# Optimization experiments

Measured on AMD Instinct MI355X. Metric: run time of the kernel, lower is better.

The kernel has to match this reference:

```python
import jax, jax.numpy as jnp
import numpy as np

B, S, D = 4, 2048, 1024
HEADS, KEY_SIZE, SIZE_PER_HEAD = 16, 64, 64
OUT_DIM = HEADS * SIZE_PER_HEAD
NEG_BIG = 1e10


def setup_inputs() -> dict:
    key = jax.random.key(0)
    ks = jax.random.split(key, 6)
    q_value = jax.random.normal(ks[0], (B, S, D), dtype=jnp.float32)
    k_value = jax.random.normal(ks[1], (B, S, D), dtype=jnp.float32)
    v_value = jax.random.normal(ks[2], (B, S, D), dtype=jnp.float32)
    v_mask = jnp.ones((B, S, 1), dtype=jnp.float32)
    q_mask = jnp.ones((B, S, 1), dtype=jnp.float32)
    scale = 1.0 / np.sqrt(D)
    Wq = jax.random.normal(ks[3], (D, HEADS * KEY_SIZE), dtype=jnp.float32) * scale
    Wk = jax.random.normal(ks[4], (D, HEADS * KEY_SIZE), dtype=jnp.float32) * scale
    Wv = jax.random.normal(ks[5], (D, OUT_DIM), dtype=jnp.float32) * scale
    return {"q_value": q_value, "k_value": k_value, "v_value": v_value,
            "v_mask": v_mask, "q_mask": q_mask, "Wq": Wq, "Wk": Wk, "Wv": Wv}


def reference(q_value, k_value, v_value, v_mask, q_mask, Wq, Wk, Wv):
    b, sq, _ = q_value.shape
    sk = k_value.shape[1]
    # projections (no bias) -> [B, S, H, dh]
    qw = (q_value @ Wq).reshape(b, sq, HEADS, KEY_SIZE)
    kw = (k_value @ Wk).reshape(b, sk, HEADS, KEY_SIZE)
    vw = (v_value @ Wv).reshape(b, sk, HEADS, SIZE_PER_HEAD)
    # scores [B, H, Sq, Sk], scaled by sqrt(key_size)
    scores = jnp.einsum('bqhd,bkhd->bhqk', qw, kw) / jnp.sqrt(
        jnp.asarray(KEY_SIZE, dtype=qw.dtype))
    # additive key-side mask: v_mask [B, Sk, 1] -> broadcast over heads/queries
    scores = scores - (1.0 - v_mask[:, None, None, :, 0]) * NEG_BIG
    attn = jax.nn.softmax(scores, axis=-1)
    out = jnp.einsum('bhqk,bkhd->bqhd', attn, vw).reshape(b, sq, OUT_DIM)
    # multiplicative query-side mask
    return out * q_mask
```

## Files before the change

kernel.cpp:

```cpp
#include <hip/hip_runtime.h>

typedef __bf16 bf16_t;
typedef __bf16 bf16x8 __attribute__((ext_vector_type(8)));
typedef __bf16 bf16x4 __attribute__((ext_vector_type(4)));
typedef __bf16 bf16x2 __attribute__((ext_vector_type(2)));
typedef float  f32x4  __attribute__((ext_vector_type(4)));
typedef float  f32x16 __attribute__((ext_vector_type(16)));
typedef unsigned int u32x4 __attribute__((ext_vector_type(4)));
typedef int i32x2 __attribute__((ext_vector_type(2)));

#define MFMA16(A, B, C) __builtin_amdgcn_mfma_f32_16x16x32_bf16((A), (B), (C), 0, 0, 0)
#define MFMA32(A, B, C) __builtin_amdgcn_mfma_f32_32x32x16_bf16((A), (B), (C), 0, 0, 0)

constexpr int BB = 4;
constexpr int SS = 2048;
constexpr int DD = 1024;
constexpr int HH = 16;
constexpr int DH = 64;
constexpr float C1 = 0.18033688011112042f;

__device__ __forceinline__ void async_copy16(const void* g, void* l) {
    __builtin_amdgcn_global_load_lds(
        (const __attribute__((address_space(1))) void*)g,
        (__attribute__((address_space(3))) void*)l, 16, 0, 0);
}

__device__ __forceinline__ unsigned pack_bf16(float lo, float hi) {
    bf16x2 t;
    t[0] = (bf16_t)lo;
    t[1] = (bf16_t)hi;
    return __builtin_bit_cast(unsigned, t);
}

__device__ __forceinline__ void permswap(unsigned& a, unsigned& b) {
    i32x2 r = __builtin_amdgcn_permlane32_swap((int)a, (int)b, false, false);
    a = (unsigned)r[0];
    b = (unsigned)r[1];
}

__global__ __launch_bounds__(256) void conv_kernel(
    const float* __restrict__ q, const float* __restrict__ k,
    const float* __restrict__ v, bf16_t* __restrict__ outb)
{
    const float* src = blockIdx.z == 0 ? q : blockIdx.z == 1 ? k : v;
    bf16_t* dst = outb + ((size_t)blockIdx.z << 23);
    size_t i = ((size_t)blockIdx.x * 256 + threadIdx.x) * 8;
    f32x4 a = *(const f32x4*)&src[i];
    f32x4 b = *(const f32x4*)&src[i + 4];
    bf16x8 o;
    o[0] = (bf16_t)a[0]; o[1] = (bf16_t)a[1]; o[2] = (bf16_t)a[2]; o[3] = (bf16_t)a[3];
    o[4] = (bf16_t)b[0]; o[5] = (bf16_t)b[1]; o[6] = (bf16_t)b[2]; o[7] = (bf16_t)b[3];
    *(bf16x8*)&dst[i] = o;
}

__global__ __launch_bounds__(256) void wtrans_kernel(
    const float* __restrict__ Wq, const float* __restrict__ Wk,
    const float* __restrict__ Wv, bf16_t* __restrict__ Wt)
{
    const float* W = blockIdx.z == 0 ? Wq : blockIdx.z == 1 ? Wk : Wv;
    bf16_t* T = Wt + ((size_t)blockIdx.z << 20);

    __shared__ __align__(16) bf16_t tile[64][72];

    const int k0 = blockIdx.x * 64;
    const int n0 = blockIdx.y * 64;
    const int tid = threadIdx.x;

    #pragma unroll
    for (int i = 0; i < 4; i++) {
        int idx = tid + i * 256;
        int kk = idx >> 4;
        int nn = (idx & 15) * 4;
        f32x4 w = *(const f32x4*)&W[(size_t)(k0 + kk) * 1024 + n0 + nn];
        tile[nn + 0][kk] = (bf16_t)w[0];
        tile[nn + 1][kk] = (bf16_t)w[1];
        tile[nn + 2][kk] = (bf16_t)w[2];
        tile[nn + 3][kk] = (bf16_t)w[3];
    }
    __syncthreads();
    #pragma unroll
    for (int i = 0; i < 2; i++) {
        int idx = tid + i * 256;
        int nn = idx >> 3;
        int kk = (idx & 7) * 8;
        *(bf16x8*)&T[(size_t)(n0 + nn) * 1024 + k0 + kk] =
            *(const bf16x8*)&tile[nn][kk];
    }
}

__global__ __launch_bounds__(256) void proj_kernel(
    const bf16_t* __restrict__ Ab, const bf16_t* __restrict__ Wt,
    bf16_t* __restrict__ qw, bf16_t* __restrict__ kw, bf16_t* __restrict__ vwt)
{
    const int which = blockIdx.z;
    const bf16_t* A = Ab + ((size_t)which << 23);
    const bf16_t* T = Wt + ((size_t)which << 20);

    __shared__ bf16_t Alds[128 * 64];
    __shared__ bf16_t Blds[128 * 64];

    const int tid = threadIdx.x;
    const int lane = tid & 63;
    const int wave = tid >> 6;
    const int quad = lane >> 4;
    const int l16 = lane & 15;

    const int id = blockIdx.x;
    const int xg = id & 7;
    const int sl = id >> 3;
    const int m0 = (((xg << 3) | (sl >> 3))) * 128;
    const int n0 = (sl & 7) * 128;

    const int wm = (wave >> 1) * 64;
    const int wn = (wave & 1) * 64;

    const int srow = lane >> 3;
    const int schk = lane & 7;

    f32x4 zero4 = {0.f, 0.f, 0.f, 0.f};
    f32x4 acc[4][4];
    #pragma unroll
    for (int i = 0; i < 4; i++)
        #pragma unroll
        for (int j = 0; j < 4; j++) acc[i][j] = zero4;

    for (int k0 = 0; k0 < DD; k0 += 64) {
        #pragma unroll
        for (int j = 0; j < 4; j++) {
            int r0 = wave * 32 + j * 8;
            int row = r0 + srow;
            int c = schk ^ (row & 7);
            async_copy16(&A[(size_t)(m0 + row) * 1024 + k0 + c * 8], &Alds[r0 * 64]);
        }
        #pragma unroll
        for (int j = 0; j < 4; j++) {
            int r0 = wave * 32 + j * 8;
            int row = r0 + srow;
            int c = schk ^ (row & 7);
            async_copy16(&T[(size_t)(n0 + row) * 1024 + k0 + c * 8], &Blds[r0 * 64]);
        }
        __syncthreads();

        #pragma unroll
        for (int s = 0; s < 2; s++) {
            bf16x8 af[4], bfr[4];
            #pragma unroll
            for (int mi = 0; mi < 4; mi++)
                af[mi] = *(const bf16x8*)&Alds[(wm + mi * 16 + l16) * 64 +
                             (((s * 4 + quad) ^ (l16 & 7)) << 3)];
            #pragma unroll
            for (int ni = 0; ni < 4; ni++)
                bfr[ni] = *(const bf16x8*)&Blds[(wn + ni * 16 + l16) * 64 +
                              (((s * 4 + quad) ^ (l16 & 7)) << 3)];
            #pragma unroll
            for (int mi = 0; mi < 4; mi++)
                #pragma unroll
                for (int ni = 0; ni < 4; ni++)
                    acc[mi][ni] = MFMA16(af[mi], bfr[ni], acc[mi][ni]);
        }
        __syncthreads();
    }

    if (which < 2) {
        bf16_t* Cout = which == 0 ? qw : kw;
        #pragma unroll
        for (int mi = 0; mi < 4; mi++)
            #pragma unroll
            for (int ni = 0; ni < 4; ni++)
                #pragma unroll
                for (int r = 0; r < 4; r++) {
                    int row = m0 + wm + mi * 16 + quad * 4 + r;
                    int col = n0 + wn + ni * 16 + l16;
                    Cout[(size_t)row * 1024 + col] = (bf16_t)acc[mi][ni][r];
                }
    } else {
        #pragma unroll
        for (int mi = 0; mi < 4; mi++)
            #pragma unroll
            for (int ni = 0; ni < 4; ni++) {
                int s0 = m0 + wm + mi * 16 + quad * 4;
                int col = n0 + wn + ni * 16 + l16;
                int b = s0 >> 11, s = s0 & 2047;
                int h = col >> 6, d = col & 63;
                bf16x4 p;
                p[0] = (bf16_t)acc[mi][ni][0]; p[1] = (bf16_t)acc[mi][ni][1];
                p[2] = (bf16_t)acc[mi][ni][2]; p[3] = (bf16_t)acc[mi][ni][3];
                *(bf16x4*)&vwt[(((size_t)((b * HH + h) * DH + d)) << 11) + s] = p;
            }
    }
}

__global__ __launch_bounds__(256) void attn_kernel(
    const bf16_t* __restrict__ qw, const bf16_t* __restrict__ kw,
    const bf16_t* __restrict__ vwt, const float* __restrict__ v_mask,
    const float* __restrict__ q_mask, float* __restrict__ out)
{
    const int linear = blockIdx.x;
    const int xg = linear & 7;
    const int sl = linear >> 3;
    const int grp = (xg << 3) | (sl >> 4);
    const int qt = sl & 15;
    const int b = grp >> 4;
    const int h = grp & 15;

    __shared__ __align__(16) bf16_t KV[4 * 4096];
    __shared__ float vml[2][64];

    const int tid = threadIdx.x;
    const int lane = tid & 63;
    const int wave = tid >> 6;
    const int l5 = lane & 31;
    const int hi = lane >> 5;
    const int q0 = qt * 128 + wave * 32;

    const int srow = lane >> 3;
    const int schk = lane & 7;

    bf16x8 qf[4];
    #pragma unroll
    for (int c = 0; c < 4; ++c)
        qf[c] = *(const bf16x8*)&qw[(size_t)(b * SS + q0 + l5) * 1024 + h * 64 +
                                    c * 16 + hi * 8];

    f32x16 zero16;
    #pragma unroll
    for (int i = 0; i < 16; ++i) zero16[i] = 0.f;

    const int vkh = (l5 & 7) ^ hi;
    const bf16_t* pj[4];
    #pragma unroll
    for (int j = 0; j < 4; ++j)
        pj[j] = &KV[l5 * 64 + ((vkh ^ (2 * j)) << 3)];
    const float* vmlp = &vml[0][hi * 4];

    const bf16_t* gk[2];
    const bf16_t* gv[2];
    #pragma unroll
    for (int j = 0; j < 2; ++j) {
        int row = (wave * 2 + j) * 8 + srow;
        int ck = schk ^ (row & 7);
        gk[j] = &kw[(size_t)(b * SS + row) * 1024 + h * 64 + ck * 8];
        gv[j] = &vwt[(((size_t)((b * HH + h) * DH + row)) << 11) + ck * 8];
    }
    const float* vmp = v_mask + b * SS + tid;

    auto stage = [&](int bi) {
        #pragma unroll
        for (int j = 0; j < 2; ++j) {
            async_copy16(gk[j], &KV[bi * 4096 + (wave * 2 + j) * 512]);
            gk[j] += 64 * 1024;
        }
        #pragma unroll
        for (int j = 0; j < 2; ++j) {
            async_copy16(gv[j], &KV[8192 + bi * 4096 + (wave * 2 + j) * 512]);
            gv[j] += 64;
        }
        if (tid < 64)
            vml[bi][tid] = (1.0f - *vmp) * 1.4426950408889634e10f;
        vmp += 64;
    };

    stage(0);
    __syncthreads();

    f32x16 o0 = zero16, o1 = zero16;
    f32x4 l4 = {0.f, 0.f, 0.f, 0.f};

    for (int t2 = 0; t2 < 32; t2 += 2) {
        #pragma unroll
        for (int cur = 0; cur < 2; ++cur) {
            if (t2 + cur + 1 < 32) stage(cur ^ 1);

            __builtin_amdgcn_s_setprio(1);
            f32x16 st0, st1;
            {
                bf16x8 k0 = *(const bf16x8*)(pj[0] + cur * 4096);
                bf16x8 k1 = *(const bf16x8*)(pj[0] + cur * 4096 + 2048);
                st0 = MFMA32(k0, qf[0], zero16);
                st1 = MFMA32(k1, qf[0], zero16);
            }
            #pragma unroll
            for (int c = 1; c < 4; ++c) {
                bf16x8 k0 = *(const bf16x8*)(pj[c] + cur * 4096);
                bf16x8 k1 = *(const bf16x8*)(pj[c] + cur * 4096 + 2048);
                st0 = MFMA32(k0, qf[c], st0);
                st1 = MFMA32(k1, qf[c], st1);
            }
            __builtin_amdgcn_s_setprio(0);

            #pragma unroll
            for (int kb = 0; kb < 2; ++kb) {
                f32x16& st = kb ? st1 : st0;
                #pragma unroll
                for (int g = 0; g < 4; ++g) {
                    f32x4 vm4 = *(const f32x4*)(vmlp + cur * 64 + kb * 32 + g * 8);
                    #pragma unroll
                    for (int j = 0; j < 4; ++j) {
                        float p = __builtin_amdgcn_exp2f(
                            __builtin_fmaf(st[g * 4 + j], C1, -vm4[j]));
                        st[g * 4 + j] = p;
                        l4[j] += p;
                    }
                }
                unsigned a0 = pack_bf16(st[0],  st[1]);
                unsigned a1 = pack_bf16(st[2],  st[3]);
                unsigned a2 = pack_bf16(st[4],  st[5]);
                unsigned a3 = pack_bf16(st[6],  st[7]);
                unsigned a4 = pack_bf16(st[8],  st[9]);
                unsigned a5 = pack_bf16(st[10], st[11]);
                unsigned a6 = pack_bf16(st[12], st[13]);
                unsigned a7 = pack_bf16(st[14], st[15]);
                permswap(a0, a2);
                permswap(a1, a3);
                permswap(a4, a6);
                permswap(a5, a7);
                u32x4 w0 = {a0, a1, a2, a3};
                u32x4 w1 = {a4, a5, a6, a7};
                bf16x8 bp0 = __builtin_bit_cast(bf16x8, w0);
                bf16x8 bp1 = __builtin_bit_cast(bf16x8, w1);

                __builtin_amdgcn_s_setprio(1);
                #pragma unroll
                for (int c = 0; c < 2; ++c) {
                    bf16x8 bp = c ? bp1 : bp0;
                    const bf16_t* pv = pj[kb * 2 + c] + 8192 + cur * 4096;
                    bf16x8 av0 = *(const bf16x8*)(pv);
                    bf16x8 av1 = *(const bf16x8*)(pv + 2048);
                    o0 = MFMA32(av0, bp, o0);
                    o1 = MFMA32(av1, bp, o1);
                }
                __builtin_amdgcn_s_setprio(0);
            }
            __syncthreads();
        }
    }

    float l_i = (l4[0] + l4[1]) + (l4[2] + l4[3]);
    l_i += __shfl_xor(l_i, 32);

    const int q = q0 + l5;
    const float sc = q_mask[b * SS + q] / l_i;
    #pragma unroll
    for (int db = 0; db < 2; ++db) {
        const f32x16 oa = db ? o1 : o0;
        #pragma unroll
        for (int g = 0; g < 4; ++g) {
            f32x4 o4;
            o4[0] = oa[g * 4 + 0] * sc;
            o4[1] = oa[g * 4 + 1] * sc;
            o4[2] = oa[g * 4 + 2] * sc;
            o4[3] = oa[g * 4 + 3] * sc;
            *(f32x4*)&out[(size_t)(b * SS + q) * 1024 + h * 64 +
                          db * 32 + g * 8 + hi * 4] = o4;
        }
    }
}

extern "C" void kernel_launch(void* const* d_in, const int* in_sizes, int n_in,
                              void* d_out, int out_size, void* d_ws, size_t ws_size,
                              hipStream_t stream)
{
    const float* q  = (const float*)d_in[0];
    const float* k  = (const float*)d_in[1];
    const float* v  = (const float*)d_in[2];
    const float* vm = (const float*)d_in[3];
    const float* qm = (const float*)d_in[4];
    const float* Wq = (const float*)d_in[5];
    const float* Wk = (const float*)d_in[6];
    const float* Wv = (const float*)d_in[7];
    float* out = (float*)d_out;

    const size_t elems = (size_t)BB * SS * DD;
    bf16_t* Ab  = (bf16_t*)d_ws;
    bf16_t* qw  = Ab + 3 * elems;
    bf16_t* kw  = qw + elems;
    bf16_t* vwt = kw + elems;
    bf16_t* Wt  = vwt + elems;

    conv_kernel<<<dim3(4096, 1, 3), 256, 0, stream>>>(q, k, v, Ab);
    wtrans_kernel<<<dim3(16, 16, 3), 256, 0, stream>>>(Wq, Wk, Wv, Wt);
    proj_kernel<<<dim3(512, 1, 3), 256, 0, stream>>>(Ab, Wt, qw, kw, vwt);
    attn_kernel<<<dim3(1024, 1, 1), 256, 0, stream>>>(qw, kw, vwt, vm, qm, out);
}
```

Before: 317.0 us.

## Shrink attention blocks to two waves with single-buffered staggered K/V staging

The attention kernel now runs 128-thread blocks covering 64 queries each, so the grid doubles to 2048 blocks. The double-buffered K/V tiles become single K and V buffers, which halves shared memory per block. V is loaded while QK^T and exp run, and the next K is loaded while PV runs, with two barriers per tile. The aim is higher occupancy and smaller LDS per block, at the cost of less K/V reuse per block, twice the global K/V traffic, and extra synchronisation.

```diff
diff --git a/kernel.cpp b/kernel.cpp
--- a/kernel.cpp
+++ b/kernel.cpp
@@ -190,7 +190,7 @@
     }
 }
 
-__global__ __launch_bounds__(256) void attn_kernel(
+__global__ __launch_bounds__(128) void attn_kernel(
     const bf16_t* __restrict__ qw, const bf16_t* __restrict__ kw,
     const bf16_t* __restrict__ vwt, const float* __restrict__ v_mask,
     const float* __restrict__ q_mask, float* __restrict__ out)
@@ -198,12 +198,12 @@
     const int linear = blockIdx.x;
     const int xg = linear & 7;
     const int sl = linear >> 3;
-    const int grp = (xg << 3) | (sl >> 4);
-    const int qt = sl & 15;
+    const int grp = (xg << 3) | (sl >> 5);
+    const int qt = sl & 31;
     const int b = grp >> 4;
     const int h = grp & 15;
 
-    __shared__ __align__(16) bf16_t KV[4 * 4096];
+    __shared__ __align__(16) bf16_t KV[2 * 4096];
     __shared__ float vml[2][64];
 
     const int tid = threadIdx.x;
@@ -211,7 +211,7 @@
     const int wave = tid >> 6;
     const int l5 = lane & 31;
     const int hi = lane >> 5;
-    const int q0 = qt * 128 + wave * 32;
+    const int q0 = qt * 64 + wave * 32;
 
     const int srow = lane >> 3;
     const int schk = lane & 7;
@@ -233,34 +233,33 @@
         pj[j] = &KV[l5 * 64 + ((vkh ^ (2 * j)) << 3)];
     const float* vmlp = &vml[0][hi * 4];
 
-    const bf16_t* gk[2];
-    const bf16_t* gv[2];
-    #pragma unroll
-    for (int j = 0; j < 2; ++j) {
-        int row = (wave * 2 + j) * 8 + srow;
-        int ck = schk ^ (row & 7);
-        gk[j] = &kw[(size_t)(b * SS + row) * 1024 + h * 64 + ck * 8];
-        gv[j] = &vwt[(((size_t)((b * HH + h) * DH + row)) << 11) + ck * 8];
-    }
+    const int ck = schk ^ srow;
+    const bf16_t* gk = &kw[(size_t)(b * SS + wave * 32 + srow) * 1024 +
+                           h * 64 + ck * 8];
+    const bf16_t* gv = &vwt[(((size_t)((b * HH + h) * DH + wave * 32 + srow)) << 11) +
+                            ck * 8];
     const float* vmp = v_mask + b * SS + tid;
 
-    auto stage = [&](int bi) {
-        #pragma unroll
-        for (int j = 0; j < 2; ++j) {
-            async_copy16(gk[j], &KV[bi * 4096 + (wave * 2 + j) * 512]);
-            gk[j] += 64 * 1024;
-        }
-        #pragma unroll
-        for (int j = 0; j < 2; ++j) {
-            async_copy16(gv[j], &KV[8192 + bi * 4096 + (wave * 2 + j) * 512]);
-            gv[j] += 64;
-        }
+    auto stageK = [&]() {
+        #pragma unroll
+        for (int j = 0; j < 4; ++j)
+            async_copy16(gk + j * 8192, &KV[(wave * 32 + j * 8) * 64]);
+        gk += 64 * 1024;
+    };
+    auto stageV = [&]() {
+        #pragma unroll
+        for (int j = 0; j < 4; ++j)
+            async_copy16(gv + j * 16384, &KV[4096 + (wave * 32 + j * 8) * 64]);
+        gv += 64;
+    };
+    auto stageVml = [&](int bi) {
         if (tid < 64)
             vml[bi][tid] = (1.0f - *vmp) * 1.4426950408889634e10f;
         vmp += 64;
     };
 
-    stage(0);
+    stageK();
+    stageVml(0);
     __syncthreads();
 
     f32x16 o0 = zero16, o1 = zero16;
@@ -269,20 +268,21 @@
     for (int t2 = 0; t2 < 32; t2 += 2) {
         #pragma unroll
         for (int cur = 0; cur < 2; ++cur) {
-            if (t2 + cur + 1 < 32) stage(cur ^ 1);
+            const int t = t2 + cur;
+            stageV();
 
             __builtin_amdgcn_s_setprio(1);
             f32x16 st0, st1;
             {
-                bf16x8 k0 = *(const bf16x8*)(pj[0] + cur * 4096);
-                bf16x8 k1 = *(const bf16x8*)(pj[0] + cur * 4096 + 2048);
+                bf16x8 k0 = *(const bf16x8*)(pj[0]);
+                bf16x8 k1 = *(const bf16x8*)(pj[0] + 2048);
                 st0 = MFMA32(k0, qf[0], zero16);
                 st1 = MFMA32(k1, qf[0], zero16);
             }
             #pragma unroll
             for (int c = 1; c < 4; ++c) {
-                bf16x8 k0 = *(const bf16x8*)(pj[c] + cur * 4096);
-                bf16x8 k1 = *(const bf16x8*)(pj[c] + cur * 4096 + 2048);
+                bf16x8 k0 = *(const bf16x8*)(pj[c]);
+                bf16x8 k1 = *(const bf16x8*)(pj[c] + 2048);
                 st0 = MFMA32(k0, qf[c], st0);
                 st1 = MFMA32(k1, qf[c], st1);
             }
@@ -302,6 +302,18 @@
                         l4[j] += p;
                     }
                 }
+            }
+
+            __syncthreads();
+
+            if (t < 31) {
+                stageK();
+                stageVml((cur ^ 1) & 1);
+            }
+
+            #pragma unroll
+            for (int kb = 0; kb < 2; ++kb) {
+                f32x16& st = kb ? st1 : st0;
                 unsigned a0 = pack_bf16(st[0],  st[1]);
                 unsigned a1 = pack_bf16(st[2],  st[3]);
                 unsigned a2 = pack_bf16(st[4],  st[5]);
@@ -323,7 +335,7 @@
                 #pragma unroll
                 for (int c = 0; c < 2; ++c) {
                     bf16x8 bp = c ? bp1 : bp0;
-                    const bf16_t* pv = pj[kb * 2 + c] + 8192 + cur * 4096;
+                    const bf16_t* pv = pj[kb * 2 + c] + 4096;
                     bf16x8 av0 = *(const bf16x8*)(pv);
                     bf16x8 av1 = *(const bf16x8*)(pv + 2048);
                     o0 = MFMA32(av0, bp, o0);
@@ -331,6 +343,7 @@
                 }
                 __builtin_amdgcn_s_setprio(0);
             }
+
             __syncthreads();
         }
     }
@@ -380,5 +393,5 @@
     conv_kernel<<<dim3(4096, 1, 3), 256, 0, stream>>>(q, k, v, Ab);
     wtrans_kernel<<<dim3(16, 16, 3), 256, 0, stream>>>(Wq, Wk, Wv, Wt);
     proj_kernel<<<dim3(512, 1, 3), 256, 0, stream>>>(Ab, Wt, qw, kw, vwt);
-    attn_kernel<<<dim3(1024, 1, 1), 256, 0, stream>>>(qw, kw, vwt, vm, qm, out);
-}
+    attn_kernel<<<dim3(2048, 1, 1), 128, 0, stream>>>(qw, kw, vwt, vm, qm, out);
+}
```

Result: slower. 349.1 us (+10.1%).

## Split attention waves into query-pair by key-half groups with LDS reduction

Applied to the files above, without the earlier changes.

Each wave now owns 64 queries (two 32-row blocks) and one 32-key half of every KV tile, instead of 32 queries over all keys. Each K fragment is reused for two query blocks, which halves LDS reads per MFMA. The per-wave partial outputs and row sums are combined through LDS at the end. The v_mask is now read straight from global inside the loop instead of being staged into shared memory. The cost is more accumulator registers (four f32x16 plus two Q sets) and an extra reduction and sync in the epilogue, which may lower occupancy.

```diff
diff --git a/kernel.cpp b/kernel.cpp
--- a/kernel.cpp
+++ b/kernel.cpp
@@ -18,6 +18,7 @@
 constexpr int HH = 16;
 constexpr int DH = 64;
 constexpr float C1 = 0.18033688011112042f;
+constexpr float C2 = 1.4426950408889634e10f;
 
 __device__ __forceinline__ void async_copy16(const void* g, void* l) {
     __builtin_amdgcn_global_load_lds(
@@ -36,6 +37,25 @@
     i32x2 r = __builtin_amdgcn_permlane32_swap((int)a, (int)b, false, false);
     a = (unsigned)r[0];
     b = (unsigned)r[1];
+}
+
+__device__ __forceinline__ void packP(const f32x16& st, bf16x8& w0, bf16x8& w1) {
+    unsigned a0 = pack_bf16(st[0],  st[1]);
+    unsigned a1 = pack_bf16(st[2],  st[3]);
+    unsigned a2 = pack_bf16(st[4],  st[5]);
+    unsigned a3 = pack_bf16(st[6],  st[7]);
+    unsigned a4 = pack_bf16(st[8],  st[9]);
+    unsigned a5 = pack_bf16(st[10], st[11]);
+    unsigned a6 = pack_bf16(st[12], st[13]);
+    unsigned a7 = pack_bf16(st[14], st[15]);
+    permswap(a0, a2);
+    permswap(a1, a3);
+    permswap(a4, a6);
+    permswap(a5, a7);
+    u32x4 u0 = {a0, a1, a2, a3};
+    u32x4 u1 = {a4, a5, a6, a7};
+    w0 = __builtin_bit_cast(bf16x8, u0);
+    w1 = __builtin_bit_cast(bf16x8, u1);
 }
 
 __global__ __launch_bounds__(256) void conv_kernel(
@@ -204,154 +224,176 @@
     const int h = grp & 15;
 
     __shared__ __align__(16) bf16_t KV[4 * 4096];
-    __shared__ float vml[2][64];
+    __shared__ float lred[2][2][64];
 
     const int tid = threadIdx.x;
     const int lane = tid & 63;
     const int wave = tid >> 6;
+    const int qg = wave >> 1;
+    const int kh = wave & 1;
     const int l5 = lane & 31;
     const int hi = lane >> 5;
-    const int q0 = qt * 128 + wave * 32;
+    const int q0 = qt * 128 + qg * 64;
 
     const int srow = lane >> 3;
     const int schk = lane & 7;
-
-    bf16x8 qf[4];
+    const int ck = schk ^ srow;
+
+    bf16x8 qf[2][4];
+    #pragma unroll
+    for (int qb = 0; qb < 2; ++qb)
+        #pragma unroll
+        for (int c = 0; c < 4; ++c)
+            qf[qb][c] = *(const bf16x8*)&qw[(size_t)(b * SS + q0 + qb * 32 + l5) * 1024 +
+                                            h * 64 + c * 16 + hi * 8];
+
+    f32x16 zero16;
+    #pragma unroll
+    for (int i = 0; i < 16; ++i) zero16[i] = 0.f;
+
+    const int vkh = (l5 & 7) ^ hi;
+    const bf16_t* pk[4];
     #pragma unroll
     for (int c = 0; c < 4; ++c)
-        qf[c] = *(const bf16x8*)&qw[(size_t)(b * SS + q0 + l5) * 1024 + h * 64 +
-                                    c * 16 + hi * 8];
-
-    f32x16 zero16;
-    #pragma unroll
-    for (int i = 0; i < 16; ++i) zero16[i] = 0.f;
-
-    const int vkh = (l5 & 7) ^ hi;
-    const bf16_t* pj[4];
-    #pragma unroll
-    for (int j = 0; j < 4; ++j)
-        pj[j] = &KV[l5 * 64 + ((vkh ^ (2 * j)) << 3)];
-    const float* vmlp = &vml[0][hi * 4];
-
-    const bf16_t* gk[2];
-    const bf16_t* gv[2];
-    #pragma unroll
-    for (int j = 0; j < 2; ++j) {
-        int row = (wave * 2 + j) * 8 + srow;
-        int ck = schk ^ (row & 7);
-        gk[j] = &kw[(size_t)(b * SS + row) * 1024 + h * 64 + ck * 8];
-        gv[j] = &vwt[(((size_t)((b * HH + h) * DH + row)) << 11) + ck * 8];
-    }
-    const float* vmp = v_mask + b * SS + tid;
+        pk[c] = &KV[kh * 2048 + l5 * 64 + ((vkh ^ (2 * c)) << 3)];
+    const bf16_t* pv[2];
+    #pragma unroll
+    for (int ks = 0; ks < 2; ++ks)
+        pv[ks] = &KV[8192 + l5 * 64 + ((vkh ^ (4 * kh) ^ (2 * ks)) << 3)];
+
+    const bf16_t* gk = &kw[(size_t)(b * SS + wave * 16 + srow) * 1024 + h * 64 + ck * 8];
+    const bf16_t* gv = &vwt[(((size_t)((b * HH + h) * DH + wave * 16 + srow)) << 11) +
+                            ck * 8];
+    const float* pvm = v_mask + b * SS + kh * 32 + hi * 4;
 
     auto stage = [&](int bi) {
         #pragma unroll
-        for (int j = 0; j < 2; ++j) {
-            async_copy16(gk[j], &KV[bi * 4096 + (wave * 2 + j) * 512]);
-            gk[j] += 64 * 1024;
-        }
-        #pragma unroll
-        for (int j = 0; j < 2; ++j) {
-            async_copy16(gv[j], &KV[8192 + bi * 4096 + (wave * 2 + j) * 512]);
-            gv[j] += 64;
-        }
-        if (tid < 64)
-            vml[bi][tid] = (1.0f - *vmp) * 1.4426950408889634e10f;
-        vmp += 64;
+        for (int j = 0; j < 2; ++j)
+            async_copy16(gk + j * 8192, &KV[bi * 4096 + (wave * 16 + j * 8) * 64]);
+        gk += 64 * 1024;
+        #pragma unroll
+        for (int j = 0; j < 2; ++j)
+            async_copy16(gv + j * 16384, &KV[8192 + bi * 4096 + (wave * 16 + j * 8) * 64]);
+        gv += 64;
     };
 
     stage(0);
     __syncthreads();
 
-    f32x16 o0 = zero16, o1 = zero16;
-    f32x4 l4 = {0.f, 0.f, 0.f, 0.f};
+    f32x16 o00 = zero16, o01 = zero16, o10 = zero16, o11 = zero16;
+    f32x4 la = {0.f, 0.f, 0.f, 0.f};
+    f32x4 lb = {0.f, 0.f, 0.f, 0.f};
 
     for (int t2 = 0; t2 < 32; t2 += 2) {
         #pragma unroll
         for (int cur = 0; cur < 2; ++cur) {
-            if (t2 + cur + 1 < 32) stage(cur ^ 1);
+            const int t = t2 + cur;
+
+            f32x4 vm4[4];
+            #pragma unroll
+            for (int g = 0; g < 4; ++g)
+                vm4[g] = *(const f32x4*)(pvm + g * 8);
+            pvm += 64;
+
+            if (t < 31) stage(cur ^ 1);
 
             __builtin_amdgcn_s_setprio(1);
             f32x16 st0, st1;
             {
-                bf16x8 k0 = *(const bf16x8*)(pj[0] + cur * 4096);
-                bf16x8 k1 = *(const bf16x8*)(pj[0] + cur * 4096 + 2048);
-                st0 = MFMA32(k0, qf[0], zero16);
-                st1 = MFMA32(k1, qf[0], zero16);
+                bf16x8 kf = *(const bf16x8*)(pk[0] + cur * 4096);
+                st0 = MFMA32(kf, qf[0][0], zero16);
+                st1 = MFMA32(kf, qf[1][0], zero16);
             }
             #pragma unroll
             for (int c = 1; c < 4; ++c) {
-                bf16x8 k0 = *(const bf16x8*)(pj[c] + cur * 4096);
-                bf16x8 k1 = *(const bf16x8*)(pj[c] + cur * 4096 + 2048);
-                st0 = MFMA32(k0, qf[c], st0);
-                st1 = MFMA32(k1, qf[c], st1);
+                bf16x8 kf = *(const bf16x8*)(pk[c] + cur * 4096);
+                st0 = MFMA32(kf, qf[0][c], st0);
+                st1 = MFMA32(kf, qf[1][c], st1);
             }
             __builtin_amdgcn_s_setprio(0);
 
             #pragma unroll
-            for (int kb = 0; kb < 2; ++kb) {
-                f32x16& st = kb ? st1 : st0;
+            for (int g = 0; g < 4; ++g) {
+                #pragma unroll
+                for (int j = 0; j < 4; ++j) {
+                    float nv = __builtin_fmaf(vm4[g][j], C2, -C2);
+                    float p0 = __builtin_amdgcn_exp2f(
+                        __builtin_fmaf(st0[g * 4 + j], C1, nv));
+                    st0[g * 4 + j] = p0;
+                    la[j] += p0;
+                    float p1 = __builtin_amdgcn_exp2f(
+                        __builtin_fmaf(st1[g * 4 + j], C1, nv));
+                    st1[g * 4 + j] = p1;
+                    lb[j] += p1;
+                }
+            }
+
+            bf16x8 bp00, bp01, bp10, bp11;
+            packP(st0, bp00, bp01);
+            packP(st1, bp10, bp11);
+
+            __builtin_amdgcn_s_setprio(1);
+            #pragma unroll
+            for (int ks = 0; ks < 2; ++ks) {
+                bf16x8 bpa = ks ? bp01 : bp00;
+                bf16x8 bpb = ks ? bp11 : bp10;
+                bf16x8 av0 = *(const bf16x8*)(pv[ks] + cur * 4096);
+                bf16x8 av1 = *(const bf16x8*)(pv[ks] + cur * 4096 + 2048);
+                o00 = MFMA32(av0, bpa, o00);
+                o10 = MFMA32(av0, bpb, o10);
+                o01 = MFMA32(av1, bpa, o01);
+                o11 = MFMA32(av1, bpb, o11);
+            }
+            __builtin_amdgcn_s_setprio(0);
+
+            __syncthreads();
+        }
+    }
+
+    float ls0 = (la[0] + la[1]) + (la[2] + la[3]);
+    float ls1 = (lb[0] + lb[1]) + (lb[2] + lb[3]);
+    float* R = (float*)KV;
+
+    if (kh == 1) {
+        *(f32x16*)&R[((qg * 2 + 0) * 2 + 0) * 1024 + lane * 16] = o00;
+        *(f32x16*)&R[((qg * 2 + 0) * 2 + 1) * 1024 + lane * 16] = o01;
+        *(f32x16*)&R[((qg * 2 + 1) * 2 + 0) * 1024 + lane * 16] = o10;
+        *(f32x16*)&R[((qg * 2 + 1) * 2 + 1) * 1024 + lane * 16] = o11;
+        lred[qg][0][lane] = ls0;
+        lred[qg][1][lane] = ls1;
+    }
+    __syncthreads();
+    if (kh == 0) {
+        o00 += *(const f32x16*)&R[((qg * 2 + 0) * 2 + 0) * 1024 + lane * 16];
+        o01 += *(const f32x16*)&R[((qg * 2 + 0) * 2 + 1) * 1024 + lane * 16];
+        o10 += *(const f32x16*)&R[((qg * 2 + 1) * 2 + 0) * 1024 + lane * 16];
+        o11 += *(const f32x16*)&R[((qg * 2 + 1) * 2 + 1) * 1024 + lane * 16];
+        ls0 += lred[qg][0][lane];
+        ls1 += lred[qg][1][lane];
+        ls0 += __shfl_xor(ls0, 32);
+        ls1 += __shfl_xor(ls1, 32);
+
+        const float sc0 = q_mask[b * SS + q0 + l5] / ls0;
+        const float sc1 = q_mask[b * SS + q0 + 32 + l5] / ls1;
+
+        #pragma unroll
+        for (int qb = 0; qb < 2; ++qb) {
+            const float sc = qb ? sc1 : sc0;
+            const int q = q0 + qb * 32 + l5;
+            #pragma unroll
+            for (int db = 0; db < 2; ++db) {
+                const f32x16 oa = qb ? (db ? o11 : o10) : (db ? o01 : o00);
                 #pragma unroll
                 for (int g = 0; g < 4; ++g) {
-                    f32x4 vm4 = *(const f32x4*)(vmlp + cur * 64 + kb * 32 + g * 8);
-                    #pragma unroll
-                    for (int j = 0; j < 4; ++j) {
-                        float p = __builtin_amdgcn_exp2f(
-                            __builtin_fmaf(st[g * 4 + j], C1, -vm4[j]));
-                        st[g * 4 + j] = p;
-                        l4[j] += p;
-                    }
+                    f32x4 o4;
+                    o4[0] = oa[g * 4 + 0] * sc;
+                    o4[1] = oa[g * 4 + 1] * sc;
+                    o4[2] = oa[g * 4 + 2] * sc;
+                    o4[3] = oa[g * 4 + 3] * sc;
+                    *(f32x4*)&out[(size_t)(b * SS + q) * 1024 + h * 64 +
+                                  db * 32 + g * 8 + hi * 4] = o4;
                 }
-                unsigned a0 = pack_bf16(st[0],  st[1]);
-                unsigned a1 = pack_bf16(st[2],  st[3]);
-                unsigned a2 = pack_bf16(st[4],  st[5]);
-                unsigned a3 = pack_bf16(st[6],  st[7]);
-                unsigned a4 = pack_bf16(st[8],  st[9]);
-                unsigned a5 = pack_bf16(st[10], st[11]);
-                unsigned a6 = pack_bf16(st[12], st[13]);
-                unsigned a7 = pack_bf16(st[14], st[15]);
-                permswap(a0, a2);
-                permswap(a1, a3);
-                permswap(a4, a6);
-                permswap(a5, a7);
-                u32x4 w0 = {a0, a1, a2, a3};
-                u32x4 w1 = {a4, a5, a6, a7};
-                bf16x8 bp0 = __builtin_bit_cast(bf16x8, w0);
-                bf16x8 bp1 = __builtin_bit_cast(bf16x8, w1);
-
-                __builtin_amdgcn_s_setprio(1);
-                #pragma unroll
-                for (int c = 0; c < 2; ++c) {
-                    bf16x8 bp = c ? bp1 : bp0;
-                    const bf16_t* pv = pj[kb * 2 + c] + 8192 + cur * 4096;
-                    bf16x8 av0 = *(const bf16x8*)(pv);
-                    bf16x8 av1 = *(const bf16x8*)(pv + 2048);
-                    o0 = MFMA32(av0, bp, o0);
-                    o1 = MFMA32(av1, bp, o1);
-                }
-                __builtin_amdgcn_s_setprio(0);
-            }
-            __syncthreads();
-        }
-    }
-
-    float l_i = (l4[0] + l4[1]) + (l4[2] + l4[3]);
-    l_i += __shfl_xor(l_i, 32);
-
-    const int q = q0 + l5;
-    const float sc = q_mask[b * SS + q] / l_i;
-    #pragma unroll
-    for (int db = 0; db < 2; ++db) {
-        const f32x16 oa = db ? o1 : o0;
-        #pragma unroll
-        for (int g = 0; g < 4; ++g) {
-            f32x4 o4;
-            o4[0] = oa[g * 4 + 0] * sc;
-            o4[1] = oa[g * 4 + 1] * sc;
-            o4[2] = oa[g * 4 + 2] * sc;
-            o4[3] = oa[g * 4 + 3] * sc;
-            *(f32x4*)&out[(size_t)(b * SS + q) * 1024 + h * 64 +
-                          db * 32 + g * 8 + hi * 4] = o4;
+            }
         }
     }
 }
```

Result: slower. 328.3 us (+3.6%).

## Fuse fp32-to-bf16 input conversion into projection GEMM tile loads

Applied to the files above, without the earlier changes.

Drops the separate conversion kernel that wrote bf16 copies of q/k/v. The projection kernel now reads fp32 activations directly, converts them in registers and writes the swizzled bf16 tile into LDS. This removes one launch and a full write plus re-read of the bf16 intermediate. In exchange, the A operand moves from async global-to-LDS copies to synchronous register loads, and each fp32 tile, twice the bytes of bf16, is fetched again by every N-block.

```diff
diff --git a/kernel.cpp b/kernel.cpp
--- a/kernel.cpp
+++ b/kernel.cpp
@@ -36,21 +36,6 @@
     i32x2 r = __builtin_amdgcn_permlane32_swap((int)a, (int)b, false, false);
     a = (unsigned)r[0];
     b = (unsigned)r[1];
-}
-
-__global__ __launch_bounds__(256) void conv_kernel(
-    const float* __restrict__ q, const float* __restrict__ k,
-    const float* __restrict__ v, bf16_t* __restrict__ outb)
-{
-    const float* src = blockIdx.z == 0 ? q : blockIdx.z == 1 ? k : v;
-    bf16_t* dst = outb + ((size_t)blockIdx.z << 23);
-    size_t i = ((size_t)blockIdx.x * 256 + threadIdx.x) * 8;
-    f32x4 a = *(const f32x4*)&src[i];
-    f32x4 b = *(const f32x4*)&src[i + 4];
-    bf16x8 o;
-    o[0] = (bf16_t)a[0]; o[1] = (bf16_t)a[1]; o[2] = (bf16_t)a[2]; o[3] = (bf16_t)a[3];
-    o[4] = (bf16_t)b[0]; o[5] = (bf16_t)b[1]; o[6] = (bf16_t)b[2]; o[7] = (bf16_t)b[3];
-    *(bf16x8*)&dst[i] = o;
 }
 
 __global__ __launch_bounds__(256) void wtrans_kernel(
@@ -89,11 +74,12 @@
 }
 
 __global__ __launch_bounds__(256) void proj_kernel(
-    const bf16_t* __restrict__ Ab, const bf16_t* __restrict__ Wt,
+    const float* __restrict__ Aq, const float* __restrict__ Ak,
+    const float* __restrict__ Av, const bf16_t* __restrict__ Wt,
     bf16_t* __restrict__ qw, bf16_t* __restrict__ kw, bf16_t* __restrict__ vwt)
 {
     const int which = blockIdx.z;
-    const bf16_t* A = Ab + ((size_t)which << 23);
+    const float* A = which == 0 ? Aq : which == 1 ? Ak : Av;
     const bf16_t* T = Wt + ((size_t)which << 20);
 
     __shared__ bf16_t Alds[128 * 64];
@@ -130,14 +116,22 @@
             int r0 = wave * 32 + j * 8;
             int row = r0 + srow;
             int c = schk ^ (row & 7);
-            async_copy16(&A[(size_t)(m0 + row) * 1024 + k0 + c * 8], &Alds[r0 * 64]);
+            async_copy16(&T[(size_t)(n0 + row) * 1024 + k0 + c * 8], &Blds[r0 * 64]);
         }
         #pragma unroll
         for (int j = 0; j < 4; j++) {
             int r0 = wave * 32 + j * 8;
             int row = r0 + srow;
             int c = schk ^ (row & 7);
-            async_copy16(&T[(size_t)(n0 + row) * 1024 + k0 + c * 8], &Blds[r0 * 64]);
+            const float* src = &A[(size_t)(m0 + row) * 1024 + k0 + c * 8];
+            f32x4 a0 = *(const f32x4*)src;
+            f32x4 a1 = *(const f32x4*)(src + 4);
+            bf16x8 o;
+            o[0] = (bf16_t)a0[0]; o[1] = (bf16_t)a0[1];
+            o[2] = (bf16_t)a0[2]; o[3] = (bf16_t)a0[3];
+            o[4] = (bf16_t)a1[0]; o[5] = (bf16_t)a1[1];
+            o[6] = (bf16_t)a1[2]; o[7] = (bf16_t)a1[3];
+            *(bf16x8*)&Alds[row * 64 + schk * 8] = o;
         }
         __syncthreads();
 
@@ -371,14 +365,12 @@
     float* out = (float*)d_out;
 
     const size_t elems = (size_t)BB * SS * DD;
-    bf16_t* Ab  = (bf16_t*)d_ws;
-    bf16_t* qw  = Ab + 3 * elems;
+    bf16_t* qw  = (bf16_t*)d_ws;
     bf16_t* kw  = qw + elems;
     bf16_t* vwt = kw + elems;
     bf16_t* Wt  = vwt + elems;
 
-    conv_kernel<<<dim3(4096, 1, 3), 256, 0, stream>>>(q, k, v, Ab);
     wtrans_kernel<<<dim3(16, 16, 3), 256, 0, stream>>>(Wq, Wk, Wv, Wt);
-    proj_kernel<<<dim3(512, 1, 3), 256, 0, stream>>>(Ab, Wt, qw, kw, vwt);
+    proj_kernel<<<dim3(512, 1, 3), 256, 0, stream>>>(q, k, v, Wt, qw, kw, vwt);
     attn_kernel<<<dim3(1024, 1, 1), 256, 0, stream>>>(qw, kw, vwt, vm, qm, out);
 }
```

New measurement: 325.1 us. 1.03x slower.
